# Kernel tuning notes

Measured on AMD Instinct MI355X. Metric: run time of the kernel, lower is better.

Reference implementation:

```python
import jax, jax.numpy as jnp
import numpy as np

B, G, K, KD = 16384, 17, 12, 16      # batch, games, kicks/game, kick feature dim
DK, DM, H, T = 16, 32, 2, 4          # d_kick, d_model, n_attn_heads, n_targets
SD, H1, H2, HH = 64, 256, 128, 32    # static_dim, backbone hidden dims, head hidden
AO = H * DM                          # attention output dim = 64
EPS = 1e-5
NEG_INF = float('-inf')


def setup_inputs() -> dict:
    ks = jax.random.split(jax.random.key(0), 18)
    n = lambda i, s, sc=0.05: jax.random.normal(ks[i], s, jnp.float32) * sc
    x_static = jax.random.normal(ks[0], (B, SD), jnp.float32)
    x_kicks = jax.random.normal(ks[1], (B, G, K, KD), jnp.float32)
    # masks: True = real game / kick; force position 0 valid so no row is fully padded
    outer_mask = jax.random.bernoulli(ks[2], 0.9, (B, G)).at[:, 0].set(True)
    inner_mask = jax.random.bernoulli(ks[3], 0.85, (B, G, K)).at[:, :, 0].set(True)
    return dict(
        x_static=x_static, x_kicks=x_kicks,
        W_ke=n(4, (KD, DK)), b_ke=jnp.zeros((DK,), jnp.float32),
        q_inner=n(5, (1, DK), 0.02),
        W_ge=n(6, (DK, DM)), b_ge=jnp.zeros((DM,), jnp.float32),
        pos_emb=n(7, (G, DM), 0.02),
        q_outer=n(8, (T * H, DM), 0.02),
        log_temp=jnp.zeros((T,), jnp.float32),
        ln_g=jnp.ones((T, AO), jnp.float32), ln_b=jnp.zeros((T, AO), jnp.float32),
        W1=n(9, (SD, H1)), b1=jnp.zeros((H1,), jnp.float32),
        g1=jnp.ones((H1,), jnp.float32), be1=jnp.zeros((H1,), jnp.float32),
        m1=n(10, (H1,)), v1=jax.random.uniform(ks[11], (H1,), jnp.float32) + 0.5,
        W2=n(12, (H1, H2)), b2=jnp.zeros((H2,), jnp.float32),
        g2=jnp.ones((H2,), jnp.float32), be2=jnp.zeros((H2,), jnp.float32),
        m2=n(13, (H2,)), v2=jax.random.uniform(ks[14], (H2,), jnp.float32) + 0.5,
        Wh1=n(15, (T, H2 + AO, HH)), bh1=jnp.zeros((T, HH), jnp.float32),
        Wh2=n(16, (T, HH)), bh2=jnp.zeros((T,), jnp.float32),
        outer_mask=outer_mask, inner_mask=inner_mask)


def _forward(x_static, x_kicks, W_ke, b_ke, q_inner, W_ge, b_ge, pos_emb,
             q_outer, log_temp, ln_g, ln_b, W1, b1, g1, be1, m1, v1,
             W2, b2, g2, be2, m2, v2, Wh1, bh1, Wh2, bh2,
             outer_mask, inner_mask):
    # kick encoder: Linear -> ReLU, [B,G,K,KD] -> [B,G,K,DK]
    kick_enc = jax.nn.relu(jnp.einsum('bgkd,de->bgke', x_kicks, W_ke) + b_ke)
    # inner AttentionPool: single learned query over kicks within each game
    ai = jnp.einsum('d,bgkd->bgk', q_inner[0], kick_enc) * (DK ** -0.5)
    ai = jnp.where(inner_mask, ai, NEG_INF)
    wi = jnp.nan_to_num(jax.nn.softmax(ai, axis=-1))       # all-masked rows -> 0
    per_game = jnp.einsum('bgk,bgkd->bgd', wi, kick_enc)   # [B,G,DK]
    # game encoder + learned positional embedding
    encoded = jax.nn.relu(per_game @ W_ge + b_ge) + pos_emb[None]  # [B,G,DM]
    # outer AttentionPool: T*H learned queries over games, per-target temperature
    ao = jnp.einsum('qd,bgd->bqg', q_outer, encoded) * (DM ** -0.5)
    ao = ao * jnp.repeat(jnp.exp(-log_temp), H)[None, :, None]
    ao = jnp.where(outer_mask[:, None, :], ao, NEG_INF)
    wo = jnp.nan_to_num(jax.nn.softmax(ao, axis=-1))
    pooled = jnp.einsum('bqg,bgd->bqd', wo, encoded).reshape(-1, T, AO)  # [B,T,64]
    # per-target LayerNorm on history vector
    mu = pooled.mean(-1, keepdims=True)
    var = ((pooled - mu) ** 2).mean(-1, keepdims=True)
    hist = (pooled - mu) * jax.lax.rsqrt(var + EPS) * ln_g[None] + ln_b[None]
    # backbone: Linear -> BatchNorm(eval) -> ReLU, x2 (dropout = identity in eval)
    z = jax.nn.relu((x_static @ W1 + b1 - m1) * jax.lax.rsqrt(v1 + EPS) * g1 + be1)
    z = jax.nn.relu((z @ W2 + b2 - m2) * jax.lax.rsqrt(v2 + EPS) * g2 + be2)
    # per-target heads on [shared_static ; history_vec]
    head_in = jnp.concatenate(
        [jnp.broadcast_to(z[:, None, :], (z.shape[0], T, H2)), hist], axis=-1)  # [B,T,192]
    h = jax.nn.relu(jnp.einsum('btd,tdh->bth', head_in, Wh1) + bh1[None])
    out = jnp.einsum('bth,th->bt', h, Wh2) + bh2[None]
    return jnp.maximum(out, 0.0)  # all targets non-negative (clamp, not softplus)


def reference(x_static, x_kicks, W_ke, b_ke, q_inner, W_ge, b_ge, pos_emb,
              q_outer, log_temp, ln_g, ln_b, W1, b1, g1, be1, m1, v1,
              W2, b2, g2, be2, m2, v2, Wh1, bh1, Wh2, bh2,
              outer_mask, inner_mask):
    return _forward(x_static, x_kicks, W_ke, b_ke, q_inner, W_ge, b_ge, pos_emb,
                    q_outer, log_temp, ln_g, ln_b, W1, b1, g1, be1, m1, v1,
                    W2, b2, g2, be2, m2, v2, Wh1, bh1, Wh2, bh2,
                    outer_mask, inner_mask)
```

## Files before the change

kernel.cpp:

```cpp
#include <hip/hip_runtime.h>
#include <math.h>

#define NEGM (-1e30f)

__device__ __forceinline__ float4 ld4(const float* p) { return *(const float4*)p; }
__device__ __forceinline__ void fma4(float4& a, float s, const float4 w) {
    a.x += s * w.x; a.y += s * w.y; a.z += s * w.z; a.w += s * w.w;
}
__device__ __forceinline__ float dot4(const float4 a, const float4 b) {
    return (a.x * b.x + a.y * b.y) + (a.z * b.z + a.w * b.w);
}
__device__ __forceinline__ void upd4(float4& p, float rm, float rw, const float4 a) {
    p.x = p.x * rm + rw * a.x; p.y = p.y * rm + rw * a.y;
    p.z = p.z * rm + rw * a.z; p.w = p.w * rm + rw * a.w;
}

__global__ __launch_bounds__(64) void hist_kernel(
    const float* __restrict__ x_kicks,
    const float* __restrict__ W_ke, const float* __restrict__ b_ke,
    const float* __restrict__ q_inner,
    const float* __restrict__ W_ge, const float* __restrict__ b_ge,
    const float* __restrict__ pos_emb, const float* __restrict__ q_outer,
    const float* __restrict__ log_temp,
    const float* __restrict__ ln_g, const float* __restrict__ ln_b,
    const int* __restrict__ outer_mask, const int* __restrict__ inner_mask,
    float* __restrict__ hist)
{
    __shared__ float s_wke[256];
    __shared__ float s_wge[512];
    __shared__ float s_qout[256];
    __shared__ float pg[17 * 20];
    __shared__ float enc[17 * 36];
    __shared__ float ao[136];

    const int lane = threadIdx.x;
    const int b    = blockIdx.x;

    *(float4*)&s_wke[lane * 4]  = ld4(W_ke + lane * 4);
    *(float4*)&s_wge[lane * 4]  = ld4(W_ge + lane * 4);
    *(float4*)&s_wge[256 + lane * 4] = ld4(W_ge + 256 + lane * 4);
    *(float4*)&s_qout[lane * 4] = ld4(q_outer + lane * 4);
    __syncthreads();

    if (lane < 51) {
        const float* xb = x_kicks + ((size_t)b * 204 + lane * 4) * 16;
        const int4 msk = *(const int4*)(inner_mask + (size_t)b * 204 + lane * 4);

        const float4 qi0 = ld4(q_inner + 0), qi1 = ld4(q_inner + 4);
        const float4 qi2 = ld4(q_inner + 8), qi3 = ld4(q_inner + 12);
        const float4 bk0 = ld4(b_ke + 0), bk1 = ld4(b_ke + 4);
        const float4 bk2 = ld4(b_ke + 8), bk3 = ld4(b_ke + 12);

        float m = NEGM, s = 0.f;
        float4 p0 = {0,0,0,0}, p1 = p0, p2 = p0, p3 = p0;

        #pragma unroll
        for (int pp = 0; pp < 4; ++pp) {
            float xs[16];
            {
                float4 x0 = ld4(xb + pp * 16 + 0), x1 = ld4(xb + pp * 16 + 4);
                float4 x2 = ld4(xb + pp * 16 + 8), x3 = ld4(xb + pp * 16 + 12);
                xs[0]=x0.x; xs[1]=x0.y; xs[2]=x0.z; xs[3]=x0.w;
                xs[4]=x1.x; xs[5]=x1.y; xs[6]=x1.z; xs[7]=x1.w;
                xs[8]=x2.x; xs[9]=x2.y; xs[10]=x2.z; xs[11]=x2.w;
                xs[12]=x3.x; xs[13]=x3.y; xs[14]=x3.z; xs[15]=x3.w;
            }
            float4 a0 = bk0, a1 = bk1, a2 = bk2, a3 = bk3;
            #pragma unroll
            for (int i = 0; i < 16; ++i) {
                float xi = xs[i];
                fma4(a0, xi, *(float4*)&s_wke[i * 16 + 0]);
                fma4(a1, xi, *(float4*)&s_wke[i * 16 + 4]);
                fma4(a2, xi, *(float4*)&s_wke[i * 16 + 8]);
                fma4(a3, xi, *(float4*)&s_wke[i * 16 + 12]);
            }
            a0.x=fmaxf(a0.x,0.f); a0.y=fmaxf(a0.y,0.f); a0.z=fmaxf(a0.z,0.f); a0.w=fmaxf(a0.w,0.f);
            a1.x=fmaxf(a1.x,0.f); a1.y=fmaxf(a1.y,0.f); a1.z=fmaxf(a1.z,0.f); a1.w=fmaxf(a1.w,0.f);
            a2.x=fmaxf(a2.x,0.f); a2.y=fmaxf(a2.y,0.f); a2.z=fmaxf(a2.z,0.f); a2.w=fmaxf(a2.w,0.f);
            a3.x=fmaxf(a3.x,0.f); a3.y=fmaxf(a3.y,0.f); a3.z=fmaxf(a3.z,0.f); a3.w=fmaxf(a3.w,0.f);

            float sc = (dot4(a0, qi0) + dot4(a1, qi1) + dot4(a2, qi2) + dot4(a3, qi3)) * 0.25f;
            int mk = (pp == 0) ? msk.x : (pp == 1) ? msk.y : (pp == 2) ? msk.z : msk.w;

            float scm = mk ? sc : NEGM;
            float mn = fmaxf(m, scm);
            float rm = __expf(m - mn);
            float rw = mk ? __expf(sc - mn) : 0.f;
            s = s * rm + rw;
            upd4(p0, rm, rw, a0); upd4(p1, rm, rw, a1);
            upd4(p2, rm, rw, a2); upd4(p3, rm, rw, a3);
            m = mn;
        }

        const int base = (lane / 3) * 3;
        float gm = fmaxf(fmaxf(__shfl(m, base), __shfl(m, base + 1)), __shfl(m, base + 2));
        float r  = __expf(m - gm);
        float sl = s * r;
        float gs = __shfl(sl, base) + __shfl(sl, base + 1) + __shfl(sl, base + 2);
        float c  = r / gs;
        p0.x*=c; p0.y*=c; p0.z*=c; p0.w*=c;
        p1.x*=c; p1.y*=c; p1.z*=c; p1.w*=c;
        p2.x*=c; p2.y*=c; p2.z*=c; p2.w*=c;
        p3.x*=c; p3.y*=c; p3.z*=c; p3.w*=c;

        float4 o0, o1, o2, o3;
        o0.x = __shfl(p0.x,base)+__shfl(p0.x,base+1)+__shfl(p0.x,base+2);
        o0.y = __shfl(p0.y,base)+__shfl(p0.y,base+1)+__shfl(p0.y,base+2);
        o0.z = __shfl(p0.z,base)+__shfl(p0.z,base+1)+__shfl(p0.z,base+2);
        o0.w = __shfl(p0.w,base)+__shfl(p0.w,base+1)+__shfl(p0.w,base+2);
        o1.x = __shfl(p1.x,base)+__shfl(p1.x,base+1)+__shfl(p1.x,base+2);
        o1.y = __shfl(p1.y,base)+__shfl(p1.y,base+1)+__shfl(p1.y,base+2);
        o1.z = __shfl(p1.z,base)+__shfl(p1.z,base+1)+__shfl(p1.z,base+2);
        o1.w = __shfl(p1.w,base)+__shfl(p1.w,base+1)+__shfl(p1.w,base+2);
        o2.x = __shfl(p2.x,base)+__shfl(p2.x,base+1)+__shfl(p2.x,base+2);
        o2.y = __shfl(p2.y,base)+__shfl(p2.y,base+1)+__shfl(p2.y,base+2);
        o2.z = __shfl(p2.z,base)+__shfl(p2.z,base+1)+__shfl(p2.z,base+2);
        o2.w = __shfl(p2.w,base)+__shfl(p2.w,base+1)+__shfl(p2.w,base+2);
        o3.x = __shfl(p3.x,base)+__shfl(p3.x,base+1)+__shfl(p3.x,base+2);
        o3.y = __shfl(p3.y,base)+__shfl(p3.y,base+1)+__shfl(p3.y,base+2);
        o3.z = __shfl(p3.z,base)+__shfl(p3.z,base+1)+__shfl(p3.z,base+2);
        o3.w = __shfl(p3.w,base)+__shfl(p3.w,base+1)+__shfl(p3.w,base+2);
        if (lane == base) {
            const int g = lane / 3;
            *(float4*)&pg[g * 20 + 0]  = o0;
            *(float4*)&pg[g * 20 + 4]  = o1;
            *(float4*)&pg[g * 20 + 8]  = o2;
            *(float4*)&pg[g * 20 + 12] = o3;
        }
    }
    __syncthreads();

    for (int t = lane; t < 136; t += 64) {
        const int g = t >> 3, dq = t & 7;
        float4 acc = ld4(b_ge + dq * 4);
        #pragma unroll
        for (int i = 0; i < 16; ++i) {
            float pv = pg[g * 20 + i];
            fma4(acc, pv, *(float4*)&s_wge[i * 32 + dq * 4]);
        }
        float4 pe = ld4(pos_emb + g * 32 + dq * 4);
        acc.x = fmaxf(acc.x, 0.f) + pe.x; acc.y = fmaxf(acc.y, 0.f) + pe.y;
        acc.z = fmaxf(acc.z, 0.f) + pe.z; acc.w = fmaxf(acc.w, 0.f) + pe.w;
        *(float4*)&enc[g * 36 + dq * 4] = acc;
    }
    __syncthreads();

    for (int t = lane; t < 136; t += 64) {
        const int q = t / 17, g = t - q * 17;
        float4 acc = {0.f, 0.f, 0.f, 0.f};
        #pragma unroll
        for (int i4 = 0; i4 < 8; ++i4) {
            float4 ev = *(float4*)&enc[g * 36 + i4 * 4];
            float4 qv = *(float4*)&s_qout[q * 32 + i4 * 4];
            acc.x += ev.x * qv.x; acc.y += ev.y * qv.y;
            acc.z += ev.z * qv.z; acc.w += ev.w * qv.w;
        }
        float sv = (acc.x + acc.y) + (acc.z + acc.w);
        sv *= 0.17677669529663687f * __expf(-log_temp[q >> 1]);
        ao[t] = outer_mask[b * 17 + g] ? sv : NEGM;
    }
    __syncthreads();

    {
        const int q = lane >> 3, j = lane & 7;
        float s0 = ao[q * 17 + j];
        float s1 = ao[q * 17 + j + 8];
        float s2 = (j == 0) ? ao[q * 17 + 16] : NEGM;
        float mx = fmaxf(fmaxf(s0, s1), s2);
        mx = fmaxf(mx, __shfl_xor(mx, 1));
        mx = fmaxf(mx, __shfl_xor(mx, 2));
        mx = fmaxf(mx, __shfl_xor(mx, 4));
        float e0 = __expf(s0 - mx), e1 = __expf(s1 - mx);
        float e2 = (j == 0) ? __expf(s2 - mx) : 0.f;
        float ssum = e0 + e1 + e2;
        ssum += __shfl_xor(ssum, 1);
        ssum += __shfl_xor(ssum, 2);
        ssum += __shfl_xor(ssum, 4);
        float inv = 1.f / ssum;
        ao[q * 17 + j] = e0 * inv;
        ao[q * 17 + j + 8] = e1 * inv;
        if (j == 0) ao[q * 17 + 16] = e2 * inv;
    }
    __syncthreads();

    {
        const int q = lane >> 3, dq = lane & 7;
        float4 acc = {0.f, 0.f, 0.f, 0.f};
        #pragma unroll
        for (int g = 0; g < 17; ++g) {
            float w = ao[q * 17 + g];
            fma4(acc, w, *(float4*)&enc[g * 36 + dq * 4]);
        }
        float sv = (acc.x + acc.y) + (acc.z + acc.w);
        sv += __shfl_xor(sv, 1); sv += __shfl_xor(sv, 2);
        sv += __shfl_xor(sv, 4); sv += __shfl_xor(sv, 8);
        float mu = sv * 0.015625f;
        float4 d;
        d.x = acc.x - mu; d.y = acc.y - mu; d.z = acc.z - mu; d.w = acc.w - mu;
        float v = (d.x * d.x + d.y * d.y) + (d.z * d.z + d.w * d.w);
        v += __shfl_xor(v, 1); v += __shfl_xor(v, 2);
        v += __shfl_xor(v, 4); v += __shfl_xor(v, 8);
        float rs = rsqrtf(v * 0.015625f + 1e-5f);
        float4 gam = ld4(ln_g + lane * 4);
        float4 bet = ld4(ln_b + lane * 4);
        float4 res;
        res.x = d.x * rs * gam.x + bet.x; res.y = d.y * rs * gam.y + bet.y;
        res.z = d.z * rs * gam.z + bet.z; res.w = d.w * rs * gam.w + bet.w;
        *(float4*)&hist[(size_t)b * 256 + lane * 4] = res;
    }
}

__global__ __launch_bounds__(256) void backbone_kernel(
    const float* __restrict__ x_static,
    const float* __restrict__ W1, const float* __restrict__ b1,
    const float* __restrict__ g1, const float* __restrict__ be1,
    const float* __restrict__ m1, const float* __restrict__ v1,
    const float* __restrict__ W2, const float* __restrict__ b2,
    const float* __restrict__ g2, const float* __restrict__ be2,
    const float* __restrict__ m2, const float* __restrict__ v2,
    const float* __restrict__ Wh1, const float* __restrict__ bh1,
    const float* __restrict__ Wh2, const float* __restrict__ bh2,
    const float* __restrict__ hist, float* __restrict__ out)
{
    __shared__ float s_x[16 * 64];
    __shared__ float s_z1[16 * 256];
    __shared__ float s_z2[16 * 132];

    const int tid = threadIdx.x;
    const int row0 = blockIdx.x * 16;

    *(float4*)&s_x[tid * 4] = ld4(x_static + (size_t)row0 * 64 + tid * 4);
    __syncthreads();

    {
        const int col = tid;
        float acc[16];
        #pragma unroll
        for (int r = 0; r < 16; ++r) acc[r] = 0.f;
        for (int k4 = 0; k4 < 16; ++k4) {
            float w0 = W1[(k4 * 4 + 0) * 256 + col];
            float w1 = W1[(k4 * 4 + 1) * 256 + col];
            float w2 = W1[(k4 * 4 + 2) * 256 + col];
            float w3 = W1[(k4 * 4 + 3) * 256 + col];
            #pragma unroll
            for (int r = 0; r < 16; ++r) {
                float4 xv = *(float4*)&s_x[r * 64 + k4 * 4];
                acc[r] += xv.x * w0 + xv.y * w1 + xv.z * w2 + xv.w * w3;
            }
        }
        float sc = rsqrtf(v1[col] + 1e-5f) * g1[col];
        float off = b1[col] - m1[col];
        float bb = be1[col];
        #pragma unroll
        for (int r = 0; r < 16; ++r)
            s_z1[r * 256 + col] = fmaxf((acc[r] + off) * sc + bb, 0.f);
    }
    __syncthreads();

    {
        const int col = tid & 127;
        const int r0 = (tid >> 7) * 8;
        float acc[8];
        #pragma unroll
        for (int r = 0; r < 8; ++r) acc[r] = 0.f;
        for (int k4 = 0; k4 < 64; ++k4) {
            float w0 = W2[(k4 * 4 + 0) * 128 + col];
            float w1 = W2[(k4 * 4 + 1) * 128 + col];
            float w2 = W2[(k4 * 4 + 2) * 128 + col];
            float w3 = W2[(k4 * 4 + 3) * 128 + col];
            #pragma unroll
            for (int r = 0; r < 8; ++r) {
                float4 zv = *(float4*)&s_z1[(r0 + r) * 256 + k4 * 4];
                acc[r] += zv.x * w0 + zv.y * w1 + zv.z * w2 + zv.w * w3;
            }
        }
        float sc = rsqrtf(v2[col] + 1e-5f) * g2[col];
        float off = b2[col] - m2[col];
        float bb = be2[col];
        #pragma unroll
        for (int r = 0; r < 8; ++r)
            s_z2[(r0 + r) * 132 + col] = fmaxf((acc[r] + off) * sc + bb, 0.f);
    }
    __syncthreads();

    {
        const int p = tid >> 2;
        const int gl = tid & 3;
        const int row = p >> 2;
        const int tgt = p & 3;
        const int j0 = gl * 8;

        float acc[8];
        #pragma unroll
        for (int j = 0; j < 8; ++j) acc[j] = bh1[tgt * 32 + j0 + j];

        const float* w1p = Wh1 + (size_t)tgt * 192 * 32 + j0;
        for (int d4 = 0; d4 < 32; ++d4) {
            float4 zv = *(float4*)&s_z2[row * 132 + d4 * 4];
            #pragma unroll
            for (int c = 0; c < 4; ++c) {
                float v = (c == 0) ? zv.x : (c == 1) ? zv.y : (c == 2) ? zv.z : zv.w;
                float4 a = ld4(w1p + (d4 * 4 + c) * 32);
                float4 bq = ld4(w1p + (d4 * 4 + c) * 32 + 4);
                acc[0] += v * a.x;  acc[1] += v * a.y;  acc[2] += v * a.z;  acc[3] += v * a.w;
                acc[4] += v * bq.x; acc[5] += v * bq.y; acc[6] += v * bq.z; acc[7] += v * bq.w;
            }
        }
        const float* hp = hist + (size_t)(row0 + row) * 256 + tgt * 64;
        const float* w1q = w1p + 128 * 32;
        for (int d4 = 0; d4 < 16; ++d4) {
            float4 hv = ld4(hp + d4 * 4);
            #pragma unroll
            for (int c = 0; c < 4; ++c) {
                float v = (c == 0) ? hv.x : (c == 1) ? hv.y : (c == 2) ? hv.z : hv.w;
                float4 a = ld4(w1q + (d4 * 4 + c) * 32);
                float4 bq = ld4(w1q + (d4 * 4 + c) * 32 + 4);
                acc[0] += v * a.x;  acc[1] += v * a.y;  acc[2] += v * a.z;  acc[3] += v * a.w;
                acc[4] += v * bq.x; acc[5] += v * bq.y; acc[6] += v * bq.z; acc[7] += v * bq.w;
            }
        }
        float ps = 0.f;
        #pragma unroll
        for (int j = 0; j < 8; ++j) ps += fmaxf(acc[j], 0.f) * Wh2[tgt * 32 + j0 + j];
        ps += __shfl_xor(ps, 1);
        ps += __shfl_xor(ps, 2);
        if (gl == 0) out[(size_t)(row0 + row) * 4 + tgt] = fmaxf(ps + bh2[tgt], 0.f);
    }
}

extern "C" void kernel_launch(void* const* d_in, const int* in_sizes, int n_in,
                              void* d_out, int out_size, void* d_ws, size_t ws_size,
                              hipStream_t stream) {
    const float* x_static = (const float*)d_in[0];
    const float* x_kicks  = (const float*)d_in[1];
    const float* W_ke     = (const float*)d_in[2];
    const float* b_ke     = (const float*)d_in[3];
    const float* q_inner  = (const float*)d_in[4];
    const float* W_ge     = (const float*)d_in[5];
    const float* b_ge     = (const float*)d_in[6];
    const float* pos_emb  = (const float*)d_in[7];
    const float* q_outer  = (const float*)d_in[8];
    const float* log_temp = (const float*)d_in[9];
    const float* ln_g     = (const float*)d_in[10];
    const float* ln_b     = (const float*)d_in[11];
    const float* W1       = (const float*)d_in[12];
    const float* b1       = (const float*)d_in[13];
    const float* g1       = (const float*)d_in[14];
    const float* be1      = (const float*)d_in[15];
    const float* m1       = (const float*)d_in[16];
    const float* v1       = (const float*)d_in[17];
    const float* W2       = (const float*)d_in[18];
    const float* b2       = (const float*)d_in[19];
    const float* g2       = (const float*)d_in[20];
    const float* be2      = (const float*)d_in[21];
    const float* m2       = (const float*)d_in[22];
    const float* v2       = (const float*)d_in[23];
    const float* Wh1      = (const float*)d_in[24];
    const float* bh1      = (const float*)d_in[25];
    const float* Wh2      = (const float*)d_in[26];
    const float* bh2      = (const float*)d_in[27];
    const int* outer_mask = (const int*)d_in[28];
    const int* inner_mask = (const int*)d_in[29];

    float* hist = (float*)d_ws;
    float* out  = (float*)d_out;

    hist_kernel<<<16384, 64, 0, stream>>>(
        x_kicks, W_ke, b_ke, q_inner, W_ge, b_ge, pos_emb, q_outer,
        log_temp, ln_g, ln_b, outer_mask, inner_mask, hist);

    backbone_kernel<<<16384 / 16, 256, 0, stream>>>(
        x_static, W1, b1, g1, be1, m1, v1, W2, b2, g2, be2, m2, v2,
        Wh1, bh1, Wh2, bh2, hist, out);
}
```

Baseline: 150.0 us.

## Compute kick encoder and inner attention pooling with fp16 MFMA

```diff
diff --git a/kernel.cpp b/kernel.cpp
--- a/kernel.cpp
+++ b/kernel.cpp
@@ -2,17 +2,14 @@
 #include <math.h>
 
 #define NEGM (-1e30f)
+
+typedef __fp16 f16x4 __attribute__((ext_vector_type(4)));
+typedef __fp16 f16x2 __attribute__((ext_vector_type(2)));
+typedef float  f32x4 __attribute__((ext_vector_type(4)));
 
 __device__ __forceinline__ float4 ld4(const float* p) { return *(const float4*)p; }
 __device__ __forceinline__ void fma4(float4& a, float s, const float4 w) {
     a.x += s * w.x; a.y += s * w.y; a.z += s * w.z; a.w += s * w.w;
-}
-__device__ __forceinline__ float dot4(const float4 a, const float4 b) {
-    return (a.x * b.x + a.y * b.y) + (a.z * b.z + a.w * b.w);
-}
-__device__ __forceinline__ void upd4(float4& p, float rm, float rw, const float4 a) {
-    p.x = p.x * rm + rw * a.x; p.y = p.y * rm + rw * a.y;
-    p.z = p.z * rm + rw * a.z; p.w = p.w * rm + rw * a.w;
 }
 
 __global__ __launch_bounds__(64) void hist_kernel(
@@ -26,138 +23,171 @@
     const int* __restrict__ outer_mask, const int* __restrict__ inner_mask,
     float* __restrict__ hist)
 {
-    __shared__ float s_wke[256];
     __shared__ float s_wge[512];
     __shared__ float s_qout[256];
     __shared__ float pg[17 * 20];
     __shared__ float enc[17 * 36];
     __shared__ float ao[136];
+    __shared__ float s_S[20];
 
     const int lane = threadIdx.x;
     const int b    = blockIdx.x;
-
-    *(float4*)&s_wke[lane * 4]  = ld4(W_ke + lane * 4);
-    *(float4*)&s_wge[lane * 4]  = ld4(W_ge + lane * 4);
+    const int jcol = lane & 15;
+    const int g    = lane >> 4;
+    const int kb   = g * 4;
+
+    *(float4*)&s_wge[lane * 4]       = ld4(W_ge + lane * 4);
     *(float4*)&s_wge[256 + lane * 4] = ld4(W_ge + 256 + lane * 4);
-    *(float4*)&s_qout[lane * 4] = ld4(q_outer + lane * 4);
-    __syncthreads();
-
-    if (lane < 51) {
-        const float* xb = x_kicks + ((size_t)b * 204 + lane * 4) * 16;
-        const int4 msk = *(const int4*)(inner_mask + (size_t)b * 204 + lane * 4);
-
-        const float4 qi0 = ld4(q_inner + 0), qi1 = ld4(q_inner + 4);
-        const float4 qi2 = ld4(q_inner + 8), qi3 = ld4(q_inner + 12);
-        const float4 bk0 = ld4(b_ke + 0), bk1 = ld4(b_ke + 4);
-        const float4 bk2 = ld4(b_ke + 8), bk3 = ld4(b_ke + 12);
-
-        float m = NEGM, s = 0.f;
-        float4 p0 = {0,0,0,0}, p1 = p0, p2 = p0, p3 = p0;
-
-        #pragma unroll
-        for (int pp = 0; pp < 4; ++pp) {
-            float xs[16];
-            {
-                float4 x0 = ld4(xb + pp * 16 + 0), x1 = ld4(xb + pp * 16 + 4);
-                float4 x2 = ld4(xb + pp * 16 + 8), x3 = ld4(xb + pp * 16 + 12);
-                xs[0]=x0.x; xs[1]=x0.y; xs[2]=x0.z; xs[3]=x0.w;
-                xs[4]=x1.x; xs[5]=x1.y; xs[6]=x1.z; xs[7]=x1.w;
-                xs[8]=x2.x; xs[9]=x2.y; xs[10]=x2.z; xs[11]=x2.w;
-                xs[12]=x3.x; xs[13]=x3.y; xs[14]=x3.z; xs[15]=x3.w;
-            }
-            float4 a0 = bk0, a1 = bk1, a2 = bk2, a3 = bk3;
-            #pragma unroll
-            for (int i = 0; i < 16; ++i) {
-                float xi = xs[i];
-                fma4(a0, xi, *(float4*)&s_wke[i * 16 + 0]);
-                fma4(a1, xi, *(float4*)&s_wke[i * 16 + 4]);
-                fma4(a2, xi, *(float4*)&s_wke[i * 16 + 8]);
-                fma4(a3, xi, *(float4*)&s_wke[i * 16 + 12]);
-            }
-            a0.x=fmaxf(a0.x,0.f); a0.y=fmaxf(a0.y,0.f); a0.z=fmaxf(a0.z,0.f); a0.w=fmaxf(a0.w,0.f);
-            a1.x=fmaxf(a1.x,0.f); a1.y=fmaxf(a1.y,0.f); a1.z=fmaxf(a1.z,0.f); a1.w=fmaxf(a1.w,0.f);
-            a2.x=fmaxf(a2.x,0.f); a2.y=fmaxf(a2.y,0.f); a2.z=fmaxf(a2.z,0.f); a2.w=fmaxf(a2.w,0.f);
-            a3.x=fmaxf(a3.x,0.f); a3.y=fmaxf(a3.y,0.f); a3.z=fmaxf(a3.z,0.f); a3.w=fmaxf(a3.w,0.f);
-
-            float sc = (dot4(a0, qi0) + dot4(a1, qi1) + dot4(a2, qi2) + dot4(a3, qi3)) * 0.25f;
-            int mk = (pp == 0) ? msk.x : (pp == 1) ? msk.y : (pp == 2) ? msk.z : msk.w;
-
-            float scm = mk ? sc : NEGM;
-            float mn = fmaxf(m, scm);
-            float rm = __expf(m - mn);
-            float rw = mk ? __expf(sc - mn) : 0.f;
-            s = s * rm + rw;
-            upd4(p0, rm, rw, a0); upd4(p1, rm, rw, a1);
-            upd4(p2, rm, rw, a2); upd4(p3, rm, rw, a3);
-            m = mn;
-        }
-
-        const int base = (lane / 3) * 3;
-        float gm = fmaxf(fmaxf(__shfl(m, base), __shfl(m, base + 1)), __shfl(m, base + 2));
-        float r  = __expf(m - gm);
-        float sl = s * r;
-        float gs = __shfl(sl, base) + __shfl(sl, base + 1) + __shfl(sl, base + 2);
-        float c  = r / gs;
-        p0.x*=c; p0.y*=c; p0.z*=c; p0.w*=c;
-        p1.x*=c; p1.y*=c; p1.z*=c; p1.w*=c;
-        p2.x*=c; p2.y*=c; p2.z*=c; p2.w*=c;
-        p3.x*=c; p3.y*=c; p3.z*=c; p3.w*=c;
-
-        float4 o0, o1, o2, o3;
-        o0.x = __shfl(p0.x,base)+__shfl(p0.x,base+1)+__shfl(p0.x,base+2);
-        o0.y = __shfl(p0.y,base)+__shfl(p0.y,base+1)+__shfl(p0.y,base+2);
-        o0.z = __shfl(p0.z,base)+__shfl(p0.z,base+1)+__shfl(p0.z,base+2);
-        o0.w = __shfl(p0.w,base)+__shfl(p0.w,base+1)+__shfl(p0.w,base+2);
-        o1.x = __shfl(p1.x,base)+__shfl(p1.x,base+1)+__shfl(p1.x,base+2);
-        o1.y = __shfl(p1.y,base)+__shfl(p1.y,base+1)+__shfl(p1.y,base+2);
-        o1.z = __shfl(p1.z,base)+__shfl(p1.z,base+1)+__shfl(p1.z,base+2);
-        o1.w = __shfl(p1.w,base)+__shfl(p1.w,base+1)+__shfl(p1.w,base+2);
-        o2.x = __shfl(p2.x,base)+__shfl(p2.x,base+1)+__shfl(p2.x,base+2);
-        o2.y = __shfl(p2.y,base)+__shfl(p2.y,base+1)+__shfl(p2.y,base+2);
-        o2.z = __shfl(p2.z,base)+__shfl(p2.z,base+1)+__shfl(p2.z,base+2);
-        o2.w = __shfl(p2.w,base)+__shfl(p2.w,base+1)+__shfl(p2.w,base+2);
-        o3.x = __shfl(p3.x,base)+__shfl(p3.x,base+1)+__shfl(p3.x,base+2);
-        o3.y = __shfl(p3.y,base)+__shfl(p3.y,base+1)+__shfl(p3.y,base+2);
-        o3.z = __shfl(p3.z,base)+__shfl(p3.z,base+1)+__shfl(p3.z,base+2);
-        o3.w = __shfl(p3.w,base)+__shfl(p3.w,base+1)+__shfl(p3.w,base+2);
-        if (lane == base) {
-            const int g = lane / 3;
-            *(float4*)&pg[g * 20 + 0]  = o0;
-            *(float4*)&pg[g * 20 + 4]  = o1;
-            *(float4*)&pg[g * 20 + 8]  = o2;
-            *(float4*)&pg[g * 20 + 12] = o3;
-        }
-    }
+    *(float4*)&s_qout[lane * 4]      = ld4(q_outer + lane * 4);
+
+    f16x4 bw;
+    #pragma unroll
+    for (int jj = 0; jj < 4; ++jj)
+        bw[jj] = (__fp16)W_ke[(kb + jj) * 16 + jcol];
+    const float bias = b_ke[jcol];
+    const f32x4 cinit = {bias, bias, bias, bias};
+    const float qv = q_inner[jcol];
+
+    const float* xb = x_kicks + (size_t)b * 204 * 16;
+    const int*   mb = inner_mask + (size_t)b * 204;
+
+    f32x4 PG   = {0.f, 0.f, 0.f, 0.f};
+    f32x4 PG16 = {0.f, 0.f, 0.f, 0.f};
+    float Sacc = 0.f, S16 = 0.f;
+
+    #pragma unroll
+    for (int t = 0; t < 12; ++t) {
+        float4 xv = ld4(xb + (16 * t + jcol) * 16 + kb);
+        f16x2 xlo = __builtin_amdgcn_cvt_pkrtz(xv.x, xv.y);
+        f16x2 xhi = __builtin_amdgcn_cvt_pkrtz(xv.z, xv.w);
+        f16x4 ax; ax[0] = xlo[0]; ax[1] = xlo[1]; ax[2] = xhi[0]; ax[3] = xhi[1];
+
+        int4 mv = *(const int4*)(mb + 16 * t + 4 * g);
+
+        f32x4 D1 = __builtin_amdgcn_mfma_f32_16x16x16f16(ax, bw, cinit, 0, 0, 0);
+        #pragma unroll
+        for (int jj = 0; jj < 4; ++jj) D1[jj] = fmaxf(D1[jj], 0.f);
+
+        f32x4 ps;
+        #pragma unroll
+        for (int jj = 0; jj < 4; ++jj) ps[jj] = D1[jj] * qv;
+        #pragma unroll
+        for (int o = 1; o < 16; o <<= 1) {
+            ps[0] += __shfl_xor(ps[0], o);
+            ps[1] += __shfl_xor(ps[1], o);
+            ps[2] += __shfl_xor(ps[2], o);
+            ps[3] += __shfl_xor(ps[3], o);
+        }
+
+        f16x4 aw;
+        #pragma unroll
+        for (int jj = 0; jj < 4; ++jj) {
+            int kk = 16 * t + 4 * g + jj;
+            int mk = (jj == 0) ? mv.x : (jj == 1) ? mv.y : (jj == 2) ? mv.z : mv.w;
+            float e = mk ? __expf(ps[jj] * 0.25f) : 0.f;
+            float w = (kk / 12 == jcol) ? e : 0.f;
+            aw[jj] = (__fp16)w;
+            Sacc += w;
+        }
+
+        f16x2 elo = __builtin_amdgcn_cvt_pkrtz(D1[0], D1[1]);
+        f16x2 ehi = __builtin_amdgcn_cvt_pkrtz(D1[2], D1[3]);
+        f16x4 be; be[0] = elo[0]; be[1] = elo[1]; be[2] = ehi[0]; be[3] = ehi[1];
+
+        PG = __builtin_amdgcn_mfma_f32_16x16x16f16(aw, be, PG, 0, 0, 0);
+    }
+
+    {
+        int kidx = 192 + jcol;
+        int kc = (kidx < 204) ? kidx : 203;
+        float4 xv = ld4(xb + kc * 16 + kb);
+        f16x2 xlo = __builtin_amdgcn_cvt_pkrtz(xv.x, xv.y);
+        f16x2 xhi = __builtin_amdgcn_cvt_pkrtz(xv.z, xv.w);
+        f16x4 ax; ax[0] = xlo[0]; ax[1] = xlo[1]; ax[2] = xhi[0]; ax[3] = xhi[1];
+
+        int km = 192 + 4 * g;
+        int kmc = (km <= 200) ? km : 200;
+        int4 mv = *(const int4*)(mb + kmc);
+
+        f32x4 D1 = __builtin_amdgcn_mfma_f32_16x16x16f16(ax, bw, cinit, 0, 0, 0);
+        #pragma unroll
+        for (int jj = 0; jj < 4; ++jj) D1[jj] = fmaxf(D1[jj], 0.f);
+
+        f32x4 ps;
+        #pragma unroll
+        for (int jj = 0; jj < 4; ++jj) ps[jj] = D1[jj] * qv;
+        #pragma unroll
+        for (int o = 1; o < 16; o <<= 1) {
+            ps[0] += __shfl_xor(ps[0], o);
+            ps[1] += __shfl_xor(ps[1], o);
+            ps[2] += __shfl_xor(ps[2], o);
+            ps[3] += __shfl_xor(ps[3], o);
+        }
+
+        f16x4 aw2;
+        #pragma unroll
+        for (int jj = 0; jj < 4; ++jj) {
+            int pos = 4 * g + jj;
+            int mk = (jj == 0) ? mv.x : (jj == 1) ? mv.y : (jj == 2) ? mv.z : mv.w;
+            bool valid = (pos < 12) && mk;
+            float e = valid ? __expf(ps[jj] * 0.25f) : 0.f;
+            float w = (jcol == 0) ? e : 0.f;
+            aw2[jj] = (__fp16)w;
+            S16 += w;
+        }
+
+        f16x2 elo = __builtin_amdgcn_cvt_pkrtz(D1[0], D1[1]);
+        f16x2 ehi = __builtin_amdgcn_cvt_pkrtz(D1[2], D1[3]);
+        f16x4 be; be[0] = elo[0]; be[1] = elo[1]; be[2] = ehi[0]; be[3] = ehi[1];
+
+        PG16 = __builtin_amdgcn_mfma_f32_16x16x16f16(aw2, be, PG16, 0, 0, 0);
+    }
+
+    Sacc += __shfl_xor(Sacc, 16);
+    Sacc += __shfl_xor(Sacc, 32);
+    S16 += __shfl_xor(S16, 16);
+    S16 += __shfl_xor(S16, 32);
+
+    if (lane < 16) s_S[lane] = Sacc;
+    if (lane == 0) s_S[16] = S16;
+    __syncthreads();
+
+    #pragma unroll
+    for (int jj = 0; jj < 4; ++jj) {
+        int game = kb + jj;
+        pg[game * 20 + jcol] = PG[jj] * (1.f / s_S[game]);
+    }
+    if (lane < 16) pg[16 * 20 + lane] = PG16[0] * (1.f / s_S[16]);
     __syncthreads();
 
     for (int t = lane; t < 136; t += 64) {
-        const int g = t >> 3, dq = t & 7;
+        const int gg = t >> 3, dq = t & 7;
         float4 acc = ld4(b_ge + dq * 4);
         #pragma unroll
         for (int i = 0; i < 16; ++i) {
-            float pv = pg[g * 20 + i];
+            float pv = pg[gg * 20 + i];
             fma4(acc, pv, *(float4*)&s_wge[i * 32 + dq * 4]);
         }
-        float4 pe = ld4(pos_emb + g * 32 + dq * 4);
+        float4 pe = ld4(pos_emb + gg * 32 + dq * 4);
         acc.x = fmaxf(acc.x, 0.f) + pe.x; acc.y = fmaxf(acc.y, 0.f) + pe.y;
         acc.z = fmaxf(acc.z, 0.f) + pe.z; acc.w = fmaxf(acc.w, 0.f) + pe.w;
-        *(float4*)&enc[g * 36 + dq * 4] = acc;
+        *(float4*)&enc[gg * 36 + dq * 4] = acc;
     }
     __syncthreads();
 
     for (int t = lane; t < 136; t += 64) {
-        const int q = t / 17, g = t - q * 17;
+        const int q = t / 17, gg = t - q * 17;
         float4 acc = {0.f, 0.f, 0.f, 0.f};
         #pragma unroll
         for (int i4 = 0; i4 < 8; ++i4) {
-            float4 ev = *(float4*)&enc[g * 36 + i4 * 4];
-            float4 qv = *(float4*)&s_qout[q * 32 + i4 * 4];
-            acc.x += ev.x * qv.x; acc.y += ev.y * qv.y;
-            acc.z += ev.z * qv.z; acc.w += ev.w * qv.w;
+            float4 ev = *(float4*)&enc[gg * 36 + i4 * 4];
+            float4 qvv = *(float4*)&s_qout[q * 32 + i4 * 4];
+            acc.x += ev.x * qvv.x; acc.y += ev.y * qvv.y;
+            acc.z += ev.z * qvv.z; acc.w += ev.w * qvv.w;
         }
         float sv = (acc.x + acc.y) + (acc.z + acc.w);
         sv *= 0.17677669529663687f * __expf(-log_temp[q >> 1]);
-        ao[t] = outer_mask[b * 17 + g] ? sv : NEGM;
+        ao[t] = outer_mask[b * 17 + gg] ? sv : NEGM;
     }
     __syncthreads();
 
@@ -187,9 +217,9 @@
         const int q = lane >> 3, dq = lane & 7;
         float4 acc = {0.f, 0.f, 0.f, 0.f};
         #pragma unroll
-        for (int g = 0; g < 17; ++g) {
-            float w = ao[q * 17 + g];
-            fma4(acc, w, *(float4*)&enc[g * 36 + dq * 4]);
+        for (int gg = 0; gg < 17; ++gg) {
+            float w = ao[q * 17 + gg];
+            fma4(acc, w, *(float4*)&enc[gg * 36 + dq * 4]);
         }
         float sv = (acc.x + acc.y) + (acc.z + acc.w);
         sv += __shfl_xor(sv, 1); sv += __shfl_xor(sv, 2);
```

Measured after the change: 145.5 us. 1.03x faster.
